# Kernel optimization log

Measured on AMD Instinct MI355X. Metric: run time of the kernel, lower is better.

## Reference

```python
import jax, jax.numpy as jnp
import numpy as np

N_NODES = 100000
N_EDGES = 1200000
N_GRAPHS = 512
N_REL = 3
NUM_SHAPES = 16
NUM_COLORS = 16
NUM_CLASS = 10


def setup_inputs() -> dict:
    key = jax.random.key(0)
    ks = jax.random.split(key, 16)
    inp = {
        "x": jax.random.randint(ks[0], (N_NODES, 2), 0, NUM_SHAPES),
        "edge_index": jax.random.randint(ks[1], (2, N_EDGES), 0, N_NODES),
        "edge_type": jax.random.randint(ks[2], (N_EDGES,), 0, N_REL),
        "batch": jnp.sort(jax.random.randint(ks[3], (N_NODES,), 0, N_GRAPHS)),
        # parameters
        "se": jax.random.normal(ks[4], (NUM_SHAPES, 8), jnp.float32) * 0.1,
        "ce": jax.random.normal(ks[5], (NUM_COLORS, 8), jnp.float32) * 0.1,
        "pre_w": jax.random.normal(ks[6], (16, 32), jnp.float32) * 0.1,
        "pre_b": jnp.zeros((32,), jnp.float32),
        "w1": jax.random.normal(ks[7], (N_REL, 32, 64), jnp.float32) * 0.1,
        "root1": jax.random.normal(ks[8], (32, 64), jnp.float32) * 0.1,
        "b1": jnp.zeros((64,), jnp.float32),
        "w2": jax.random.normal(ks[9], (N_REL, 64, 64), jnp.float32) * 0.1,
        "root2": jax.random.normal(ks[10], (64, 64), jnp.float32) * 0.1,
        "b2": jnp.zeros((64,), jnp.float32),
        "cls_w": jax.random.normal(ks[11], (64, NUM_CLASS), jnp.float32) * 0.1,
        "cls_b": jnp.zeros((NUM_CLASS,), jnp.float32),
    }
    return inp


def _rgcn(h, src, dst, edge_type, weight, root, bias):
    # PyG RGCNConv with aggr='mean': out = x @ root + bias + sum_r mean_{edges of rel r}(x_j @ W_r)
    out = h @ root + bias
    for r in range(N_REL):
        mask = (edge_type == r)
        hr = h @ weight[r]                      # [N, out] transform-then-gather
        msg = jnp.where(mask[:, None], hr[src], 0.0)  # [E, out]
        agg = jax.ops.segment_sum(msg, dst, num_segments=N_NODES)
        cnt = jax.ops.segment_sum(mask.astype(h.dtype), dst, num_segments=N_NODES)
        out = out + agg / jnp.maximum(cnt, 1.0)[:, None]
    return out


def reference(x, edge_index, edge_type, batch, se, ce, pre_w, pre_b,
              w1, root1, b1, w2, root2, b2, cls_w, cls_b):
    h = jnp.concatenate([se[x[:, 0]], ce[x[:, 1]]], axis=1)  # [N,16]
    h = jax.nn.relu(h @ pre_w + pre_b)                        # [N,32]
    src, dst = edge_index[0], edge_index[1]
    h = jax.nn.relu(_rgcn(h, src, dst, edge_type, w1, root1, b1))  # [N,64]
    h = jax.nn.relu(_rgcn(h, src, dst, edge_type, w2, root2, b2))  # [N,64]
    # global mean pool over graph ids
    s = jax.ops.segment_sum(h, batch, num_segments=N_GRAPHS)
    c = jax.ops.segment_sum(jnp.ones((h.shape[0],), h.dtype), batch, num_segments=N_GRAPHS)
    g = s / jnp.maximum(c, 1.0)[:, None]                      # [G,64]
    return g @ cls_w + cls_b                                  # [G,num_class]
```

## Files before the change

### kernel.cpp

```cpp
#include <hip/hip_runtime.h>

#define NN 100000
#define NE 1200000
#define NG 512
#define NSEG (3 * NN)
#define CHUNK 1024
#define NCHUNK ((NSEG + CHUNK - 1) / CHUNK)

typedef __bf16 bf16x8 __attribute__((ext_vector_type(8)));
typedef float f32x4 __attribute__((ext_vector_type(4)));

static constexpr size_t AGG_OFF   = 0;
static constexpr size_t AGG_BYTES = (size_t)NSEG * 32 * 4;
static constexpr size_t HIST_OFF  = AGG_OFF + AGG_BYTES;
static constexpr size_t START_OFF = HIST_OFF + (size_t)NSEG * 4;
static constexpr size_t CSUM_OFF  = START_OFF + (size_t)NSEG * 4;
static constexpr size_t ESRC_OFF  = CSUM_OFF + 4096;
static constexpr size_t POOL_OFF  = ESRC_OFF + (size_t)NE * 4;
static constexpr size_t H1_OFF    = POOL_OFF + (size_t)NG * 64 * 4;
static constexpr size_t H2_OFF    = H1_OFF + (size_t)NN * 64 * 2;
static constexpr size_t WT1H_OFF  = H2_OFF + (size_t)NN * 64 * 4;
static constexpr size_t WT1L_OFF  = WT1H_OFF + 64 * 128 * 2;
static constexpr size_t WT2H_OFF  = WT1L_OFF + 64 * 128 * 2;
static constexpr size_t WT2L_OFF  = WT2H_OFF + 64 * 256 * 2;
static constexpr size_t TAB_OFF   = WT2L_OFF + 64 * 256 * 2;
static constexpr size_t CB_OFF    = TAB_OFF + 256 * 32 * 4;
static constexpr size_t RS_OFF    = ((CB_OFF + NN + 15) / 16) * 16;

__device__ __forceinline__ void async_copy16(void* lds, const void* g) {
    __builtin_amdgcn_global_load_lds(
        (const __attribute__((address_space(1))) void*)g,
        (__attribute__((address_space(3))) void*)lds, 16, 0, 0);
}

__device__ __forceinline__ void prepw_elem(const float* root, const float* w,
                                           __bf16* wh, __bf16* wl, int cin, int t) {
    int kt = 4 * cin;
    if (t >= 64 * kt) return;
    int j = t / kt, k = t % kt;
    int sidx = k / cin, kk = k % cin;
    float v = (sidx == 0) ? root[kk * 64 + j]
                          : w[((size_t)(sidx - 1) * cin + kk) * 64 + j];
    __bf16 h = (__bf16)v;
    wh[t] = h;
    wl[t] = (__bf16)(v - (float)h);
}

__global__ __launch_bounds__(256)
void k_prep_all(const int* __restrict__ x, const float* __restrict__ se,
                const float* __restrict__ ce, const float* __restrict__ pw,
                const float* __restrict__ pb,
                const float* __restrict__ root1, const float* __restrict__ w1,
                const float* __restrict__ root2, const float* __restrict__ w2,
                __bf16* __restrict__ wh1, __bf16* __restrict__ wl1,
                __bf16* __restrict__ wh2, __bf16* __restrict__ wl2,
                float* __restrict__ table, unsigned char* __restrict__ cb) {
    int b = blockIdx.x, t = threadIdx.x;
    if (b < 32) {
        prepw_elem(root1, w1, wh1, wl1, 32, b * 256 + t);
    } else if (b < 96) {
        prepw_elem(root2, w2, wh2, wl2, 64, (b - 32) * 256 + t);
    } else if (b == 96) {
        __shared__ float sW[16 * 32];
        __shared__ float sB[32];
        for (int i = t; i < 512; i += 256) sW[i] = pw[i];
        if (t < 32) sB[t] = pb[t];
        __syncthreads();
        int cmb = t, s = cmb >> 4, c = cmb & 15;
        float in[16];
#pragma unroll
        for (int k = 0; k < 8; k++) in[k] = se[s * 8 + k];
#pragma unroll
        for (int k = 0; k < 8; k++) in[8 + k] = ce[c * 8 + k];
        float acc[32];
#pragma unroll
        for (int j = 0; j < 32; j++) acc[j] = sB[j];
#pragma unroll
        for (int k = 0; k < 16; k++) {
            float hv = in[k];
#pragma unroll
            for (int j = 0; j < 32; j++) acc[j] += hv * sW[k * 32 + j];
        }
        float* o = table + (size_t)cmb * 32;
#pragma unroll
        for (int j = 0; j < 32; j += 4)
            *(float4*)(o + j) = make_float4(fmaxf(acc[j], 0.f), fmaxf(acc[j + 1], 0.f),
                                            fmaxf(acc[j + 2], 0.f), fmaxf(acc[j + 3], 0.f));
    } else {
        int n = (b - 97) * 256 + t;
        if (n < NN) cb[n] = (unsigned char)(x[2 * n] * 16 + x[2 * n + 1]);
    }
}

__global__ __launch_bounds__(256)
void k_rank(const int* __restrict__ ei, const int* __restrict__ et,
            int* __restrict__ hist, unsigned int* __restrict__ rs) {
    int e = blockIdx.x * 256 + threadIdx.x;
    if (e >= NE) return;
    int d = ei[NE + e];
    int r = et[e];
    int seg = r * NN + d;
    unsigned int rank = (unsigned int)atomicAdd(&hist[seg], 1);
    rs[e] = (rank << 19) | (unsigned int)seg;
}

__global__ __launch_bounds__(256)
void k_chunksum(const int* __restrict__ hist, int* __restrict__ csum) {
    __shared__ int s[256];
    int b = blockIdx.x, t = threadIdx.x;
    int base = b * CHUNK + t * 4;
    int sum = 0;
#pragma unroll
    for (int k = 0; k < 4; k++) {
        int i = base + k;
        if (i < NSEG) sum += hist[i];
    }
    s[t] = sum;
    __syncthreads();
    for (int off = 128; off > 0; off >>= 1) {
        if (t < off) s[t] += s[t + off];
        __syncthreads();
    }
    if (t == 0) csum[b] = s[0];
}

__global__ __launch_bounds__(512)
void k_chunkscan(int* __restrict__ csum) {
    __shared__ int s[512];
    int t = threadIdx.x;
    int v = (t < NCHUNK) ? csum[t] : 0;
    s[t] = v;
    __syncthreads();
    for (int off = 1; off < 512; off <<= 1) {
        int x = (t >= off) ? s[t - off] : 0;
        __syncthreads();
        s[t] += x;
        __syncthreads();
    }
    if (t < NCHUNK) csum[t] = s[t] - v;
}

__global__ __launch_bounds__(256)
void k_localscan(int* __restrict__ hist_end, const int* __restrict__ csum,
                 int* __restrict__ start) {
    __shared__ int s[256];
    int b = blockIdx.x, t = threadIdx.x;
    int base = b * CHUNK + t * 4;
    int v[4];
    int s4 = 0;
#pragma unroll
    for (int k = 0; k < 4; k++) {
        int i = base + k;
        v[k] = (i < NSEG) ? hist_end[i] : 0;
        s4 += v[k];
    }
    s[t] = s4;
    __syncthreads();
    for (int off = 1; off < 256; off <<= 1) {
        int x = (t >= off) ? s[t - off] : 0;
        __syncthreads();
        s[t] += x;
        __syncthreads();
    }
    int excl = s[t] - s4 + csum[b];
#pragma unroll
    for (int k = 0; k < 4; k++) {
        int i = base + k;
        if (i < NSEG) {
            start[i] = excl;
            hist_end[i] = excl + v[k];
        }
        excl += v[k];
    }
}

__global__ __launch_bounds__(256)
void k_fill2(const int* __restrict__ ei, const unsigned char* __restrict__ cb,
             const int* __restrict__ start, const unsigned int* __restrict__ rs,
             int* __restrict__ esrc) {
    int e = blockIdx.x * 256 + threadIdx.x;
    if (e >= NE) return;
    int s = ei[e];
    unsigned int v = rs[e];
    int seg = (int)(v & 0x7FFFFu);
    int pos = start[seg] + (int)(v >> 19);
    esrc[pos] = s | ((int)cb[s] << 17);
}

__global__ __launch_bounds__(256)
void k_gather_t(const int* __restrict__ start, const int* __restrict__ end,
                const int* __restrict__ esrc, const float* __restrict__ table,
                float* __restrict__ agg) {
    int tid = blockIdx.x * 256 + threadIdx.x;
    int seg = tid >> 3;
    int p = tid & 7;
    if (seg >= NSEG) return;
    int st = start[seg], en = end[seg];
    float4 acc = make_float4(0.f, 0.f, 0.f, 0.f);
    int i = st;
    for (; i + 4 <= en; i += 4) {
        int v0 = esrc[i], v1 = esrc[i + 1], v2 = esrc[i + 2], v3 = esrc[i + 3];
        float4 a = *(const float4*)(table + ((v0 >> 17) & 0xFF) * 32 + p * 4);
        float4 b = *(const float4*)(table + ((v1 >> 17) & 0xFF) * 32 + p * 4);
        float4 c = *(const float4*)(table + ((v2 >> 17) & 0xFF) * 32 + p * 4);
        float4 d = *(const float4*)(table + ((v3 >> 17) & 0xFF) * 32 + p * 4);
        acc.x += (a.x + b.x) + (c.x + d.x);
        acc.y += (a.y + b.y) + (c.y + d.y);
        acc.z += (a.z + b.z) + (c.z + d.z);
        acc.w += (a.w + b.w) + (c.w + d.w);
    }
    for (; i < en; i++) {
        int v = esrc[i];
        float4 a = *(const float4*)(table + ((v >> 17) & 0xFF) * 32 + p * 4);
        acc.x += a.x; acc.y += a.y; acc.z += a.z; acc.w += a.w;
    }
    int c = en - st;
    float inv = 1.f / (float)(c > 1 ? c : 1);
    acc.x *= inv; acc.y *= inv; acc.z *= inv; acc.w *= inv;
    *(float4*)(agg + (size_t)seg * 32 + p * 4) = acc;
}

__global__ __launch_bounds__(256)
void k_gather64(const int* __restrict__ start, const int* __restrict__ end,
                const int* __restrict__ esrc, const __bf16* __restrict__ h,
                __bf16* __restrict__ agg) {
    int tid = blockIdx.x * 256 + threadIdx.x;
    int seg = tid >> 3;
    int p = tid & 7;
    if (seg >= NSEG) return;
    int st = start[seg], en = end[seg];
    float acc[8];
#pragma unroll
    for (int j = 0; j < 8; j++) acc[j] = 0.f;
    int i = st;
    for (; i + 4 <= en; i += 4) {
        int s0 = esrc[i] & 0x1FFFF, s1 = esrc[i + 1] & 0x1FFFF;
        int s2 = esrc[i + 2] & 0x1FFFF, s3 = esrc[i + 3] & 0x1FFFF;
        bf16x8 v0 = *(const bf16x8*)(h + (size_t)s0 * 64 + p * 8);
        bf16x8 v1 = *(const bf16x8*)(h + (size_t)s1 * 64 + p * 8);
        bf16x8 v2 = *(const bf16x8*)(h + (size_t)s2 * 64 + p * 8);
        bf16x8 v3 = *(const bf16x8*)(h + (size_t)s3 * 64 + p * 8);
#pragma unroll
        for (int j = 0; j < 8; j++)
            acc[j] += ((float)v0[j] + (float)v1[j]) + ((float)v2[j] + (float)v3[j]);
    }
    for (; i < en; i++) {
        int s = esrc[i] & 0x1FFFF;
        bf16x8 v = *(const bf16x8*)(h + (size_t)s * 64 + p * 8);
#pragma unroll
        for (int j = 0; j < 8; j++) acc[j] += (float)v[j];
    }
    int c = en - st;
    float inv = 1.f / (float)(c > 1 ? c : 1);
    bf16x8 o;
#pragma unroll
    for (int j = 0; j < 8; j++) o[j] = (__bf16)(acc[j] * inv);
    *(bf16x8*)(agg + (size_t)seg * 64 + p * 8) = o;
}

__device__ __forceinline__ void split8(float4 a0, float4 a1, bf16x8& hi, bf16x8& lo) {
    float v[8] = {a0.x, a0.y, a0.z, a0.w, a1.x, a1.y, a1.z, a1.w};
#pragma unroll
    for (int i = 0; i < 8; i++) {
        __bf16 h = (__bf16)v[i];
        hi[i] = h;
        lo[i] = (__bf16)(v[i] - (float)h);
    }
}

__global__ __launch_bounds__(256, 1)
void k_combine_l1(const float* __restrict__ table, const unsigned char* __restrict__ cb,
                  const float* __restrict__ agg,
                  const __bf16* __restrict__ wh, const __bf16* __restrict__ wl,
                  const float* __restrict__ bias, __bf16* __restrict__ h_out) {
    constexpr int KT = 128;
    __shared__ float sIN[64 * 64];
    __shared__ __bf16 sWH[64 * 64];
    __shared__ __bf16 sWL[64 * 64];

    const int tid = threadIdx.x;
    const int wave = tid >> 6;
    const int lane = tid & 63;
    const int cA = lane & 15;
    const int kg = lane >> 4;
    const int n0 = blockIdx.x * 64;

    f32x4 acc[4];
#pragma unroll
    for (int nb = 0; nb < 4; nb++) {
        float bv = bias[nb * 16 + cA];
        acc[nb][0] = bv; acc[nb][1] = bv; acc[nb][2] = bv; acc[nb][3] = bv;
    }

    for (int c = 0; c < 2; c++) {
        if (c) __syncthreads();
#pragma unroll
        for (int i = 0; i < 4; i++) {
            int F = tid + i * 256;
            int row = F >> 4, j = F & 15;
            int jor = j ^ (row & 7);
            int n = n0 + row; if (n > NN - 1) n = NN - 1;
            int sidx = 2 * c + (jor >> 3);
            int jj = jor & 7;
            const float* src = (sidx == 0)
                ? table + (size_t)cb[n] * 32 + jj * 4
                : agg + ((size_t)(sidx - 1) * NN + n) * 32 + jj * 4;
            async_copy16(sIN + (size_t)F * 4, src);
        }
#pragma unroll
        for (int i = 0; i < 2; i++) {
            int F = tid + i * 256;
            int col = F >> 3, s = F & 7;
            int sor = s ^ (col & 7);
            async_copy16(sWH + (size_t)F * 8, wh + (size_t)col * KT + c * 64 + sor * 8);
            async_copy16(sWL + (size_t)F * 8, wl + (size_t)col * KT + c * 64 + sor * 8);
        }
        __syncthreads();
#pragma unroll
        for (int ks = 0; ks < 2; ks++) {
            const int rowL = wave * 16 + cA;
            const int jA = ks * 8 + kg * 2;
            float4 a0 = ((const float4*)sIN)[rowL * 16 + (jA ^ (rowL & 7))];
            float4 a1 = ((const float4*)sIN)[rowL * 16 + ((jA + 1) ^ (rowL & 7))];
            bf16x8 ah, al;
            split8(a0, a1, ah, al);
            const int k8 = ks * 4 + kg;
#pragma unroll
            for (int nb = 0; nb < 4; nb++) {
                const int col = nb * 16 + cA;
                const int bs = col * 8 + (k8 ^ (col & 7));
                bf16x8 bh = ((const bf16x8*)sWH)[bs];
                bf16x8 bl = ((const bf16x8*)sWL)[bs];
                acc[nb] = __builtin_amdgcn_mfma_f32_16x16x32_bf16(ah, bh, acc[nb], 0, 0, 0);
                acc[nb] = __builtin_amdgcn_mfma_f32_16x16x32_bf16(al, bh, acc[nb], 0, 0, 0);
                acc[nb] = __builtin_amdgcn_mfma_f32_16x16x32_bf16(ah, bl, acc[nb], 0, 0, 0);
                acc[nb] = __builtin_amdgcn_mfma_f32_16x16x32_bf16(al, bl, acc[nb], 0, 0, 0);
            }
        }
    }
#pragma unroll
    for (int nb = 0; nb < 4; nb++) {
#pragma unroll
        for (int r = 0; r < 4; r++) {
            int n = n0 + wave * 16 + kg * 4 + r;
            if (n < NN)
                h_out[(size_t)n * 64 + nb * 16 + cA] = (__bf16)fmaxf(acc[nb][r], 0.f);
        }
    }
}

__global__ __launch_bounds__(256, 1)
void k_combine_l2(const __bf16* __restrict__ h1b, const __bf16* __restrict__ aggb,
                  const __bf16* __restrict__ wh, const __bf16* __restrict__ wl,
                  const float* __restrict__ bias, float* __restrict__ h_out) {
    constexpr int KT = 256;
    __shared__ __bf16 sINb[64 * 64];
    __shared__ __bf16 sWH[64 * 64];
    __shared__ __bf16 sWL[64 * 64];

    const int tid = threadIdx.x;
    const int wave = tid >> 6;
    const int lane = tid & 63;
    const int cA = lane & 15;
    const int kg = lane >> 4;
    const int n0 = blockIdx.x * 64;

    f32x4 acc[4];
#pragma unroll
    for (int nb = 0; nb < 4; nb++) {
        float bv = bias[nb * 16 + cA];
        acc[nb][0] = bv; acc[nb][1] = bv; acc[nb][2] = bv; acc[nb][3] = bv;
    }

    for (int c = 0; c < 4; c++) {
        if (c) __syncthreads();
#pragma unroll
        for (int i = 0; i < 2; i++) {
            int F = tid + i * 256;
            int row = F >> 3, j = F & 7;
            int jor = j ^ (row & 7);
            int n = n0 + row; if (n > NN - 1) n = NN - 1;
            const __bf16* src = (c == 0)
                ? h1b + (size_t)n * 64 + jor * 8
                : aggb + ((size_t)(c - 1) * NN + n) * 64 + jor * 8;
            async_copy16(sINb + (size_t)F * 8, src);
        }
#pragma unroll
        for (int i = 0; i < 2; i++) {
            int F = tid + i * 256;
            int col = F >> 3, s = F & 7;
            int sor = s ^ (col & 7);
            async_copy16(sWH + (size_t)F * 8, wh + (size_t)col * KT + c * 64 + sor * 8);
            async_copy16(sWL + (size_t)F * 8, wl + (size_t)col * KT + c * 64 + sor * 8);
        }
        __syncthreads();
#pragma unroll
        for (int ks = 0; ks < 2; ks++) {
            const int rowL = wave * 16 + cA;
            const int s8 = ks * 4 + kg;
            bf16x8 ah = ((const bf16x8*)sINb)[rowL * 8 + (s8 ^ (rowL & 7))];
#pragma unroll
            for (int nb = 0; nb < 4; nb++) {
                const int col = nb * 16 + cA;
                const int bs = col * 8 + (s8 ^ (col & 7));
                bf16x8 bh = ((const bf16x8*)sWH)[bs];
                bf16x8 bl = ((const bf16x8*)sWL)[bs];
                acc[nb] = __builtin_amdgcn_mfma_f32_16x16x32_bf16(ah, bh, acc[nb], 0, 0, 0);
                acc[nb] = __builtin_amdgcn_mfma_f32_16x16x32_bf16(ah, bl, acc[nb], 0, 0, 0);
            }
        }
    }
#pragma unroll
    for (int nb = 0; nb < 4; nb++) {
#pragma unroll
        for (int r = 0; r < 4; r++) {
            int n = n0 + wave * 16 + kg * 4 + r;
            if (n < NN)
                h_out[(size_t)n * 64 + nb * 16 + cA] = fmaxf(acc[nb][r], 0.f);
        }
    }
}

__global__ __launch_bounds__(256)
void k_pool(const float* __restrict__ h, const int* __restrict__ batch,
            float* __restrict__ pool) {
    int g = blockIdx.x;
    auto lb = [&](int v) {
        int lo = 0, hi = NN;
        while (lo < hi) {
            int m = (lo + hi) >> 1;
            if (batch[m] < v) lo = m + 1; else hi = m;
        }
        return lo;
    };
    int st = lb(g), en = lb(g + 1);
    int col = threadIdx.x & 63, chunk = threadIdx.x >> 6;
    float acc = 0.f;
    for (int n = st + chunk; n < en; n += 4) acc += h[(size_t)n * 64 + col];
    __shared__ float s[256];
    s[threadIdx.x] = acc;
    __syncthreads();
    if (chunk == 0) {
        float tot = s[col] + s[64 + col] + s[128 + col] + s[192 + col];
        int c = en - st;
        pool[g * 64 + col] = tot / (float)(c > 1 ? c : 1);
    }
}

__global__ __launch_bounds__(256)
void k_final(const float* __restrict__ pool, const float* __restrict__ cw,
             const float* __restrict__ cb, float* __restrict__ out) {
    int t = blockIdx.x * blockDim.x + threadIdx.x;
    if (t >= NG * 10) return;
    int g = t / 10, j = t % 10;
    float acc = 0.f;
#pragma unroll
    for (int k = 0; k < 64; k++) acc += pool[g * 64 + k] * cw[k * 10 + j];
    out[t] = cb[j] + acc;
}

extern "C" void kernel_launch(void* const* d_in, const int* in_sizes, int n_in,
                              void* d_out, int out_size, void* d_ws, size_t ws_size,
                              hipStream_t stream) {
    const int* x      = (const int*)d_in[0];
    const int* ei     = (const int*)d_in[1];
    const int* et     = (const int*)d_in[2];
    const int* batch  = (const int*)d_in[3];
    const float* se   = (const float*)d_in[4];
    const float* ce   = (const float*)d_in[5];
    const float* pw   = (const float*)d_in[6];
    const float* pb   = (const float*)d_in[7];
    const float* w1   = (const float*)d_in[8];
    const float* root1= (const float*)d_in[9];
    const float* b1   = (const float*)d_in[10];
    const float* w2   = (const float*)d_in[11];
    const float* root2= (const float*)d_in[12];
    const float* b2   = (const float*)d_in[13];
    const float* cw   = (const float*)d_in[14];
    const float* cbias= (const float*)d_in[15];
    float* out = (float*)d_out;

    char* ws = (char*)d_ws;
    float*  agg1 = (float*)(ws + AGG_OFF);
    __bf16* aggb = (__bf16*)(ws + AGG_OFF);
    int*   hist  = (int*)(ws + HIST_OFF);
    int*   start = (int*)(ws + START_OFF);
    int*   csum  = (int*)(ws + CSUM_OFF);
    int*   esrc  = (int*)(ws + ESRC_OFF);
    float* pool  = (float*)(ws + POOL_OFF);
    __bf16* h1b  = (__bf16*)(ws + H1_OFF);
    float* h2    = (float*)(ws + H2_OFF);
    __bf16* wt1h = (__bf16*)(ws + WT1H_OFF);
    __bf16* wt1l = (__bf16*)(ws + WT1L_OFF);
    __bf16* wt2h = (__bf16*)(ws + WT2H_OFF);
    __bf16* wt2l = (__bf16*)(ws + WT2L_OFF);
    float* table = (float*)(ws + TAB_OFF);
    unsigned char* cbarr = (unsigned char*)(ws + CB_OFF);
    unsigned int* rs = (unsigned int*)(ws + RS_OFF);

    (void)hipMemsetAsync(hist, 0, (size_t)NSEG * 4, stream);

    int prep_blocks = 97 + (NN + 255) / 256;
    k_prep_all<<<prep_blocks, 256, 0, stream>>>(x, se, ce, pw, pb, root1, w1, root2, w2,
                                                wt1h, wt1l, wt2h, wt2l, table, cbarr);

    k_rank<<<(NE + 255) / 256, 256, 0, stream>>>(ei, et, hist, rs);
    k_chunksum<<<NCHUNK, 256, 0, stream>>>(hist, csum);
    k_chunkscan<<<1, 512, 0, stream>>>(csum);
    k_localscan<<<NCHUNK, 256, 0, stream>>>(hist, csum, start);
    k_fill2<<<(NE + 255) / 256, 256, 0, stream>>>(ei, cbarr, start, rs, esrc);

    k_gather_t<<<(NSEG * 8 + 255) / 256, 256, 0, stream>>>(start, hist, esrc, table, agg1);
    k_combine_l1<<<(NN + 63) / 64, 256, 0, stream>>>(table, cbarr, agg1,
                                                     wt1h, wt1l, b1, h1b);
    k_gather64<<<(NSEG * 8 + 255) / 256, 256, 0, stream>>>(start, hist, esrc, h1b, aggb);
    k_combine_l2<<<(NN + 63) / 64, 256, 0, stream>>>(h1b, aggb,
                                                     wt2h, wt2l, b2, h2);

    k_pool<<<NG, 256, 0, stream>>>(h2, batch, pool);
    k_final<<<(NG * 10 + 255) / 256, 256, 0, stream>>>(pool, cw, cbias, out);
}
```

Measured before the change: 199.2 us.

## Split rank histogram into four copies and fuse prep, rank, pool and classifier

The edge-ranking atomics now go to four separate histogram copies, chosen by the edge index modulo four, to cut contention on each counter. Per-copy prefix offsets are packed into one 8-bit-field word that the fill kernel reads. Prep and rank are merged into one launch, and pooling is merged with the final classifier, removing two launches. In exchange the memset and histogram reads are four times larger, and the 8-bit offset fields would overflow if a segment held more than 255 edges in one copy.

```diff
diff --git a/kernel.cpp b/kernel.cpp
--- a/kernel.cpp
+++ b/kernel.cpp
@@ -4,6 +4,7 @@
 #define NE 1200000
 #define NG 512
 #define NSEG (3 * NN)
+#define NC 4
 #define CHUNK 1024
 #define NCHUNK ((NSEG + CHUNK - 1) / CHUNK)
 
@@ -13,11 +14,12 @@
 static constexpr size_t AGG_OFF   = 0;
 static constexpr size_t AGG_BYTES = (size_t)NSEG * 32 * 4;
 static constexpr size_t HIST_OFF  = AGG_OFF + AGG_BYTES;
-static constexpr size_t START_OFF = HIST_OFF + (size_t)NSEG * 4;
-static constexpr size_t CSUM_OFF  = START_OFF + (size_t)NSEG * 4;
+static constexpr size_t START_OFF = HIST_OFF + (size_t)NC * NSEG * 4;
+static constexpr size_t END_OFF   = START_OFF + (size_t)NSEG * 4;
+static constexpr size_t COFF_OFF  = END_OFF + (size_t)NSEG * 4;
+static constexpr size_t CSUM_OFF  = COFF_OFF + (size_t)NSEG * 4;
 static constexpr size_t ESRC_OFF  = CSUM_OFF + 4096;
-static constexpr size_t POOL_OFF  = ESRC_OFF + (size_t)NE * 4;
-static constexpr size_t H1_OFF    = POOL_OFF + (size_t)NG * 64 * 4;
+static constexpr size_t H1_OFF    = ESRC_OFF + (size_t)NE * 4;
 static constexpr size_t H2_OFF    = H1_OFF + (size_t)NN * 64 * 2;
 static constexpr size_t WT1H_OFF  = H2_OFF + (size_t)NN * 64 * 4;
 static constexpr size_t WT1L_OFF  = WT1H_OFF + 64 * 128 * 2;
@@ -46,16 +48,30 @@
     wl[t] = (__bf16)(v - (float)h);
 }
 
-__global__ __launch_bounds__(256)
-void k_prep_all(const int* __restrict__ x, const float* __restrict__ se,
-                const float* __restrict__ ce, const float* __restrict__ pw,
-                const float* __restrict__ pb,
-                const float* __restrict__ root1, const float* __restrict__ w1,
-                const float* __restrict__ root2, const float* __restrict__ w2,
-                __bf16* __restrict__ wh1, __bf16* __restrict__ wl1,
-                __bf16* __restrict__ wh2, __bf16* __restrict__ wl2,
-                float* __restrict__ table, unsigned char* __restrict__ cb) {
+#define RB_BASE 488
+__global__ __launch_bounds__(256)
+void k_rank_prep(const int* __restrict__ ei, const int* __restrict__ et,
+                 int* __restrict__ hist4, unsigned int* __restrict__ rs,
+                 const int* __restrict__ x, const float* __restrict__ se,
+                 const float* __restrict__ ce, const float* __restrict__ pw,
+                 const float* __restrict__ pb,
+                 const float* __restrict__ root1, const float* __restrict__ w1,
+                 const float* __restrict__ root2, const float* __restrict__ w2,
+                 __bf16* __restrict__ wh1, __bf16* __restrict__ wl1,
+                 __bf16* __restrict__ wh2, __bf16* __restrict__ wl2,
+                 float* __restrict__ table, unsigned char* __restrict__ cb) {
     int b = blockIdx.x, t = threadIdx.x;
+    if (b >= RB_BASE) {
+        int e = (b - RB_BASE) * 256 + t;
+        if (e >= NE) return;
+        int d = ei[NE + e];
+        int r = et[e];
+        int seg = r * NN + d;
+        int c = e & (NC - 1);
+        unsigned int rank = (unsigned int)atomicAdd(&hist4[c * NSEG + seg], 1);
+        rs[e] = (rank << 19) | (unsigned int)seg;
+        return;
+    }
     if (b < 32) {
         prepw_elem(root1, w1, wh1, wl1, 32, b * 256 + t);
     } else if (b < 96) {
@@ -93,19 +109,7 @@
 }
 
 __global__ __launch_bounds__(256)
-void k_rank(const int* __restrict__ ei, const int* __restrict__ et,
-            int* __restrict__ hist, unsigned int* __restrict__ rs) {
-    int e = blockIdx.x * 256 + threadIdx.x;
-    if (e >= NE) return;
-    int d = ei[NE + e];
-    int r = et[e];
-    int seg = r * NN + d;
-    unsigned int rank = (unsigned int)atomicAdd(&hist[seg], 1);
-    rs[e] = (rank << 19) | (unsigned int)seg;
-}
-
-__global__ __launch_bounds__(256)
-void k_chunksum(const int* __restrict__ hist, int* __restrict__ csum) {
+void k_chunksum(const int* __restrict__ hist4, int* __restrict__ csum) {
     __shared__ int s[256];
     int b = blockIdx.x, t = threadIdx.x;
     int base = b * CHUNK + t * 4;
@@ -113,7 +117,10 @@
 #pragma unroll
     for (int k = 0; k < 4; k++) {
         int i = base + k;
-        if (i < NSEG) sum += hist[i];
+        if (i < NSEG) {
+#pragma unroll
+            for (int c = 0; c < NC; c++) sum += hist4[c * NSEG + i];
+        }
     }
     s[t] = sum;
     __syncthreads();
@@ -141,18 +148,26 @@
 }
 
 __global__ __launch_bounds__(256)
-void k_localscan(int* __restrict__ hist_end, const int* __restrict__ csum,
-                 int* __restrict__ start) {
+void k_localscan(const int* __restrict__ hist4, const int* __restrict__ csum,
+                 int* __restrict__ start, int* __restrict__ end, int* __restrict__ coff) {
     __shared__ int s[256];
     int b = blockIdx.x, t = threadIdx.x;
     int base = b * CHUNK + t * 4;
-    int v[4];
+    int tot[4], cofv[4];
     int s4 = 0;
 #pragma unroll
     for (int k = 0; k < 4; k++) {
         int i = base + k;
-        v[k] = (i < NSEG) ? hist_end[i] : 0;
-        s4 += v[k];
+        int c0 = 0, c1 = 0, c2 = 0, c3 = 0;
+        if (i < NSEG) {
+            c0 = hist4[0 * NSEG + i];
+            c1 = hist4[1 * NSEG + i];
+            c2 = hist4[2 * NSEG + i];
+            c3 = hist4[3 * NSEG + i];
+        }
+        tot[k] = c0 + c1 + c2 + c3;
+        cofv[k] = c0 | ((c0 + c1) << 8) | ((c0 + c1 + c2) << 16);
+        s4 += tot[k];
     }
     s[t] = s4;
     __syncthreads();
@@ -168,22 +183,26 @@
         int i = base + k;
         if (i < NSEG) {
             start[i] = excl;
-            hist_end[i] = excl + v[k];
-        }
-        excl += v[k];
+            end[i] = excl + tot[k];
+            coff[i] = cofv[k];
+        }
+        excl += tot[k];
     }
 }
 
 __global__ __launch_bounds__(256)
 void k_fill2(const int* __restrict__ ei, const unsigned char* __restrict__ cb,
-             const int* __restrict__ start, const unsigned int* __restrict__ rs,
-             int* __restrict__ esrc) {
+             const int* __restrict__ start, const int* __restrict__ coff,
+             const unsigned int* __restrict__ rs, int* __restrict__ esrc) {
     int e = blockIdx.x * 256 + threadIdx.x;
     if (e >= NE) return;
     int s = ei[e];
     unsigned int v = rs[e];
     int seg = (int)(v & 0x7FFFFu);
-    int pos = start[seg] + (int)(v >> 19);
+    int rank = (int)(v >> 19);
+    int c = e & (NC - 1);
+    int off = c ? ((coff[seg] >> (8 * (c - 1))) & 0xFF) : 0;
+    int pos = start[seg] + off + rank;
     esrc[pos] = s | ((int)cb[s] << 17);
 }
 
@@ -422,8 +441,9 @@
 }
 
 __global__ __launch_bounds__(256)
-void k_pool(const float* __restrict__ h, const int* __restrict__ batch,
-            float* __restrict__ pool) {
+void k_pool_final(const float* __restrict__ h, const int* __restrict__ batch,
+                  const float* __restrict__ cw, const float* __restrict__ cbias,
+                  float* __restrict__ out) {
     int g = blockIdx.x;
     auto lb = [&](int v) {
         int lo = 0, hi = NN;
@@ -438,25 +458,22 @@
     float acc = 0.f;
     for (int n = st + chunk; n < en; n += 4) acc += h[(size_t)n * 64 + col];
     __shared__ float s[256];
+    __shared__ float mean[64];
     s[threadIdx.x] = acc;
     __syncthreads();
     if (chunk == 0) {
         float tot = s[col] + s[64 + col] + s[128 + col] + s[192 + col];
         int c = en - st;
-        pool[g * 64 + col] = tot / (float)(c > 1 ? c : 1);
-    }
-}
-
-__global__ __launch_bounds__(256)
-void k_final(const float* __restrict__ pool, const float* __restrict__ cw,
-             const float* __restrict__ cb, float* __restrict__ out) {
-    int t = blockIdx.x * blockDim.x + threadIdx.x;
-    if (t >= NG * 10) return;
-    int g = t / 10, j = t % 10;
-    float acc = 0.f;
-#pragma unroll
-    for (int k = 0; k < 64; k++) acc += pool[g * 64 + k] * cw[k * 10 + j];
-    out[t] = cb[j] + acc;
+        mean[col] = tot / (float)(c > 1 ? c : 1);
+    }
+    __syncthreads();
+    if (threadIdx.x < 10) {
+        int j = threadIdx.x;
+        float o = cbias[j];
+#pragma unroll
+        for (int k = 0; k < 64; k++) o += mean[k] * cw[k * 10 + j];
+        out[g * 10 + j] = o;
+    }
 }
 
 extern "C" void kernel_launch(void* const* d_in, const int* in_sizes, int n_in,
@@ -483,11 +500,12 @@
     char* ws = (char*)d_ws;
     float*  agg1 = (float*)(ws + AGG_OFF);
     __bf16* aggb = (__bf16*)(ws + AGG_OFF);
-    int*   hist  = (int*)(ws + HIST_OFF);
+    int*   hist4 = (int*)(ws + HIST_OFF);
     int*   start = (int*)(ws + START_OFF);
+    int*   end   = (int*)(ws + END_OFF);
+    int*   coff  = (int*)(ws + COFF_OFF);
     int*   csum  = (int*)(ws + CSUM_OFF);
     int*   esrc  = (int*)(ws + ESRC_OFF);
-    float* pool  = (float*)(ws + POOL_OFF);
     __bf16* h1b  = (__bf16*)(ws + H1_OFF);
     float* h2    = (float*)(ws + H2_OFF);
     __bf16* wt1h = (__bf16*)(ws + WT1H_OFF);
@@ -498,25 +516,24 @@
     unsigned char* cbarr = (unsigned char*)(ws + CB_OFF);
     unsigned int* rs = (unsigned int*)(ws + RS_OFF);
 
-    (void)hipMemsetAsync(hist, 0, (size_t)NSEG * 4, stream);
-
-    int prep_blocks = 97 + (NN + 255) / 256;
-    k_prep_all<<<prep_blocks, 256, 0, stream>>>(x, se, ce, pw, pb, root1, w1, root2, w2,
-                                                wt1h, wt1l, wt2h, wt2l, table, cbarr);
-
-    k_rank<<<(NE + 255) / 256, 256, 0, stream>>>(ei, et, hist, rs);
-    k_chunksum<<<NCHUNK, 256, 0, stream>>>(hist, csum);
+    (void)hipMemsetAsync(hist4, 0, (size_t)NC * NSEG * 4, stream);
+
+    int rank_blocks = RB_BASE + (NE + 255) / 256;
+    k_rank_prep<<<rank_blocks, 256, 0, stream>>>(ei, et, hist4, rs,
+                                                 x, se, ce, pw, pb, root1, w1, root2, w2,
+                                                 wt1h, wt1l, wt2h, wt2l, table, cbarr);
+
+    k_chunksum<<<NCHUNK, 256, 0, stream>>>(hist4, csum);
     k_chunkscan<<<1, 512, 0, stream>>>(csum);
-    k_localscan<<<NCHUNK, 256, 0, stream>>>(hist, csum, start);
-    k_fill2<<<(NE + 255) / 256, 256, 0, stream>>>(ei, cbarr, start, rs, esrc);
-
-    k_gather_t<<<(NSEG * 8 + 255) / 256, 256, 0, stream>>>(start, hist, esrc, table, agg1);
+    k_localscan<<<NCHUNK, 256, 0, stream>>>(hist4, csum, start, end, coff);
+    k_fill2<<<(NE + 255) / 256, 256, 0, stream>>>(ei, cbarr, start, coff, rs, esrc);
+
+    k_gather_t<<<(NSEG * 8 + 255) / 256, 256, 0, stream>>>(start, end, esrc, table, agg1);
     k_combine_l1<<<(NN + 63) / 64, 256, 0, stream>>>(table, cbarr, agg1,
                                                      wt1h, wt1l, b1, h1b);
-    k_gather64<<<(NSEG * 8 + 255) / 256, 256, 0, stream>>>(start, hist, esrc, h1b, aggb);
+    k_gather64<<<(NSEG * 8 + 255) / 256, 256, 0, stream>>>(start, end, esrc, h1b, aggb);
     k_combine_l2<<<(NN + 63) / 64, 256, 0, stream>>>(h1b, aggb,
                                                      wt2h, wt2l, b2, h2);
 
-    k_pool<<<NG, 256, 0, stream>>>(h2, batch, pool);
-    k_final<<<(NG * 10 + 255) / 256, 256, 0, stream>>>(pool, cw, cbias, out);
-}
+    k_pool_final<<<NG, 256, 0, stream>>>(h2, batch, cw, cbias, out);
+}
```

After: 198.2 us. About the same (-0.5%).
